# Performance work log

Hardware: AMD Instinct MI355X
Metric: run time of the kernel (lower is better)

## Reference

```python
import jax, jax.numpy as jnp
import numpy as np

U_DIM = 2048
V_DIM = 2048
LATENT = 2048
BATCH = 8192
SLOPE = 0.001  # LeakyReLU negative slope
EPS = 1e-5     # torch LayerNorm default eps


def layer_norm(x, gamma, beta):
    mu = jnp.mean(x, axis=-1, keepdims=True)
    var = jnp.var(x, axis=-1, keepdims=True)
    return (x - mu) * jax.lax.rsqrt(var + EPS) * gamma + beta


def leaky_relu(x):
    return jnp.where(x >= 0, x, SLOPE * x)


def setup_inputs() -> dict:
    key = jax.random.key(0)
    ks = jax.random.split(key, 6)
    u = jax.random.normal(ks[0], (BATCH, V_DIM), dtype=jnp.float32)
    v = jax.random.normal(ks[1], (BATCH, U_DIM), dtype=jnp.float32)
    # LayerNorm affine params (torch default: weight=1, bias=0 at init; randomize slightly)
    ln_u_w = jnp.ones((V_DIM,), jnp.float32)
    ln_u_b = jnp.zeros((V_DIM,), jnp.float32)
    ln_v_w = jnp.ones((U_DIM,), jnp.float32)
    ln_v_b = jnp.zeros((U_DIM,), jnp.float32)
    # Linear params (Kaiming-uniform-like scale)
    su = 1.0 / np.sqrt(V_DIM)
    sv = 1.0 / np.sqrt(U_DIM)
    W_u = jax.random.uniform(ks[2], (V_DIM, LATENT), jnp.float32, -su, su)
    b_u = jax.random.uniform(ks[3], (LATENT,), jnp.float32, -su, su)
    W_v = jax.random.uniform(ks[4], (U_DIM, LATENT), jnp.float32, -sv, sv)
    b_v = jax.random.uniform(ks[5], (LATENT,), jnp.float32, -sv, sv)
    return {"u": u, "v": v, "ln_u_w": ln_u_w, "ln_u_b": ln_u_b,
            "ln_v_w": ln_v_w, "ln_v_b": ln_v_b,
            "W_u": W_u, "b_u": b_u, "W_v": W_v, "b_v": b_v}


def reference(u, v, ln_u_w, ln_u_b, ln_v_w, ln_v_b, W_u, b_u, W_v, b_v):
    # u tower: LayerNorm -> Linear -> LeakyReLU
    hu = leaky_relu(layer_norm(u, ln_u_w, ln_u_b) @ W_u + b_u)   # [B, latent]
    # v tower: LayerNorm -> Linear -> LeakyReLU
    hv = leaky_relu(layer_norm(v, ln_v_w, ln_v_b) @ W_v + b_v)   # [B, latent]
    # dot-product reduction per row
    return jnp.sum(hu * hv, axis=-1)                              # [B]
```

## Files before the change

kernel.cpp:

```cpp
#include <hip/hip_runtime.h>

typedef unsigned short u16;
typedef __attribute__((ext_vector_type(8))) short short8;
typedef __attribute__((ext_vector_type(16))) float f32x16;

#define DIM 2048
#define NROWS 8192
#define SLOPE 0.001f
#define LN_EPS 1e-5f

#define LN_BLOCKS 4096
#define WT_BLOCKS 2048

#define BM 256
#define BN 256
#define BK 64
#define NT (DIM / BK)
#define TAUMAX (2 * NT)

__device__ __forceinline__ u16 f2bf(float f) {
    unsigned int u = __float_as_uint(f);
    u += 0x7FFFu + ((u >> 16) & 1u);
    return (u16)(u >> 16);
}

__device__ __forceinline__ void gload_lds16(const void* g, void* l) {
    __builtin_amdgcn_global_load_lds(
        (const __attribute__((address_space(1))) void*)g,
        (__attribute__((address_space(3))) void*)l, 16, 0, 0);
}

__global__ __launch_bounds__(256) void prep_kernel(
    const float* __restrict__ u, const float* __restrict__ v,
    const float* __restrict__ lnu_w, const float* __restrict__ lnu_b,
    const float* __restrict__ lnv_w, const float* __restrict__ lnv_b,
    const float* __restrict__ Wu, const float* __restrict__ Wv,
    u16* __restrict__ Au, u16* __restrict__ Av,
    u16* __restrict__ WtU, u16* __restrict__ WtV,
    float* __restrict__ out)
{
    __shared__ u16 tile[64][66];

    if (blockIdx.x < NROWS / 256)
        out[(blockIdx.x << 8) | threadIdx.x] = 0.f;

    if (blockIdx.x < LN_BLOCKS) {
        const int wave = threadIdx.x >> 6;
        const int lane = threadIdx.x & 63;
        const int r = blockIdx.x * 4 + wave;
        const bool isv = r >= NROWS;
        const int row = isv ? (r - NROWS) : r;
        const float* __restrict__ src = (isv ? v : u) + (size_t)row * DIM;
        const float* __restrict__ gw = isv ? lnv_w : lnu_w;
        const float* __restrict__ gb = isv ? lnv_b : lnu_b;
        u16* __restrict__ dst = (isv ? Av : Au) + (size_t)row * DIM;

        float4 x[8];
        #pragma unroll
        for (int i = 0; i < 8; ++i)
            x[i] = *(const float4*)(src + i * 256 + lane * 4);

        float s = 0.f, s2 = 0.f;
        #pragma unroll
        for (int i = 0; i < 8; ++i) {
            s  += (x[i].x + x[i].y) + (x[i].z + x[i].w);
            s2 += x[i].x*x[i].x + x[i].y*x[i].y + x[i].z*x[i].z + x[i].w*x[i].w;
        }
        #pragma unroll
        for (int m = 1; m < 64; m <<= 1) {
            s  += __shfl_xor(s, m);
            s2 += __shfl_xor(s2, m);
        }
        const float mu = s * (1.0f / DIM);
        const float rstd = rsqrtf(s2 * (1.0f / DIM) - mu * mu + LN_EPS);

        #pragma unroll
        for (int i = 0; i < 8; ++i) {
            const float4 w4 = *(const float4*)(gw + i * 256 + lane * 4);
            const float4 b4 = *(const float4*)(gb + i * 256 + lane * 4);
            union { u16 us[4]; uint2 v2; } pk;
            pk.us[0] = f2bf((x[i].x - mu) * rstd * w4.x + b4.x);
            pk.us[1] = f2bf((x[i].y - mu) * rstd * w4.y + b4.y);
            pk.us[2] = f2bf((x[i].z - mu) * rstd * w4.z + b4.z);
            pk.us[3] = f2bf((x[i].w - mu) * rstd * w4.w + b4.w);
            *(uint2*)(dst + i * 256 + lane * 4) = pk.v2;
        }
    } else {
        const int b = blockIdx.x - LN_BLOCKS;
        const int tower = b >> 10;
        const int t6 = b & 1023;
        const int n0 = (t6 & 31) * 64;
        const int k0 = (t6 >> 5) * 64;
        const float* __restrict__ src = tower ? Wv : Wu;
        u16* __restrict__ dst = tower ? WtV : WtU;
        const int c  = threadIdx.x & 15;
        const int rq = threadIdx.x >> 4;

        #pragma unroll
        for (int i = 0; i < 4; ++i) {
            const int k = rq + 16 * i;
            const float4 w = *(const float4*)(src + (size_t)(k0 + k) * DIM + n0 + c * 4);
            union { u16 us[4]; uint2 v2; } pk;
            pk.us[0] = f2bf(w.x); pk.us[1] = f2bf(w.y);
            pk.us[2] = f2bf(w.z); pk.us[3] = f2bf(w.w);
            *(uint2*)&tile[k][c * 4] = pk.v2;
        }
        __syncthreads();
        #pragma unroll
        for (int i = 0; i < 4; ++i) {
            const int n = rq + 16 * i;
            union { u16 us[4]; uint2 v2; } pk;
            #pragma unroll
            for (int j = 0; j < 4; ++j) pk.us[j] = tile[c * 4 + j][n];
            *(uint2*)(dst + (size_t)(n0 + n) * DIM + k0 + c * 4) = pk.v2;
        }
    }
}

__global__ __launch_bounds__(512) void fused_gemm_dot(
    const u16* __restrict__ Au, const u16* __restrict__ Av,
    const u16* __restrict__ WtU, const u16* __restrict__ WtV,
    const float* __restrict__ b_u, const float* __restrict__ b_v,
    uint4* __restrict__ Hu, float* __restrict__ out)
{
    __shared__ __align__(16) u16 smA[3][BM * BK];
    __shared__ __align__(16) u16 smB[2][BN * BK];

    const int tid   = threadIdx.x;
    const int wave  = tid >> 6;
    const int lane  = tid & 63;
    const int l31   = lane & 31;
    const int khalf = lane >> 5;
    const int wr    = wave >> 2;
    const int wc    = wave & 3;
    const int srow  = lane >> 3;
    const int gsw   = ((lane & 7) ^ srow ^ wave) * 8;

    const int bid = blockIdx.x;
    const int bn  = bid & 7;
    const int bm  = bid >> 3;
    const size_t arow0 = (size_t)bm * BM;
    const size_t ncol0 = (size_t)bn * BN;

#define STAGE_A(T, buf, h) do {                                                    \
        const u16* as_ = (((T) >= NT) ? Av : Au) + arow0 * DIM                     \
                         + (size_t)((T) & (NT - 1)) * BK;                          \
        _Pragma("unroll")                                                          \
        for (int i2_ = 0; i2_ < 2; ++i2_) {                                        \
            const int rg_ = (h) * 128 + i2_ * 64 + wave * 8;                       \
            gload_lds16(as_ + (size_t)(rg_ + srow) * DIM + gsw,                    \
                        &smA[buf][rg_ * BK]);                                      \
        }                                                                          \
    } while (0)

#define STAGE_B(T, h) do {                                                         \
        const u16* bs_ = (((T) >= NT) ? WtV : WtU) + ncol0 * DIM                   \
                         + (size_t)((T) & (NT - 1)) * BK;                          \
        _Pragma("unroll")                                                          \
        for (int i2_ = 0; i2_ < 2; ++i2_) {                                        \
            const int rg_ = (h) * 128 + i2_ * 64 + wave * 8;                       \
            gload_lds16(bs_ + (size_t)(rg_ + srow) * DIM + gsw,                    \
                        &smB[(T) & 1][rg_ * BK]);                                  \
        }                                                                          \
    } while (0)

#define PHASE(AB, BB, KS, STAGE_STMT) do {                                         \
        const u16* sa_ = &smA[AB][0];                                              \
        const u16* sb_ = &smB[BB][0];                                              \
        const int cb_ = (KS) * 2 + khalf;                                          \
        short8 af_[4], bf_[2];                                                     \
        _Pragma("unroll")                                                          \
        for (int mi_ = 0; mi_ < 4; ++mi_) {                                        \
            const int row_ = wr * 128 + mi_ * 32 + l31;                            \
            const int sl_ = cb_ ^ (row_ & 7) ^ ((row_ >> 3) & 7);                  \
            af_[mi_] = *(const short8*)(sa_ + row_ * BK + sl_ * 8);                \
        }                                                                          \
        _Pragma("unroll")                                                          \
        for (int ni_ = 0; ni_ < 2; ++ni_) {                                        \
            const int row_ = wc * 64 + ni_ * 32 + l31;                             \
            const int sl_ = cb_ ^ (row_ & 7) ^ ((row_ >> 3) & 7);                  \
            bf_[ni_] = *(const short8*)(sb_ + row_ * BK + sl_ * 8);                \
        }                                                                          \
        STAGE_STMT;                                                                \
        __builtin_amdgcn_s_barrier();                                              \
        asm volatile("s_waitcnt lgkmcnt(0)" ::: "memory");                         \
        __builtin_amdgcn_s_setprio(1);                                             \
        _Pragma("unroll")                                                          \
        for (int mi_ = 0; mi_ < 4; ++mi_)                                          \
            _Pragma("unroll")                                                      \
            for (int ni_ = 0; ni_ < 2; ++ni_)                                      \
                acc[mi_][ni_] = __builtin_amdgcn_mfma_f32_32x32x16_bf16(           \
                    af_[mi_], bf_[ni_], acc[mi_][ni_], 0, 0, 0);                   \
        __builtin_amdgcn_s_setprio(0);                                             \
    } while (0)

    f32x16 acc[4][2];

    #pragma unroll
    for (int mi = 0; mi < 4; ++mi)
        #pragma unroll
        for (int ni = 0; ni < 2; ++ni)
            #pragma unroll
            for (int r = 0; r < 16; ++r)
                acc[mi][ni][r] = 0.f;

    STAGE_A(0, 0, 0); STAGE_A(0, 0, 1);
    STAGE_B(0, 0);    STAGE_B(0, 1);
    STAGE_A(1, 1, 0); STAGE_A(1, 1, 1);
    asm volatile("s_waitcnt vmcnt(4)" ::: "memory");
    __builtin_amdgcn_s_barrier();
    asm volatile("" ::: "memory");

    int a0 = 0;
    #pragma unroll 1
    for (int i = 0; i < NT; ++i) {
        const int tau = 2 * i;
        const int a1 = (a0 + 1 < 3) ? a0 + 1 : a0 - 2;
        const int a2 = (a0 + 2 < 3) ? a0 + 2 : a0 - 1;

        PHASE(a0, 0, 0, { STAGE_B(tau + 1, 0); });
        __builtin_amdgcn_s_barrier();
        PHASE(a0, 0, 1, { STAGE_B(tau + 1, 1); });
        __builtin_amdgcn_s_barrier();
        PHASE(a0, 0, 2, { if (i < NT - 1) STAGE_A(tau + 2, a2, 0); });
        __builtin_amdgcn_s_barrier();
        PHASE(a0, 0, 3, { if (i < NT - 1) STAGE_A(tau + 2, a2, 1); });
        if (i < NT - 1) asm volatile("s_waitcnt vmcnt(4)" ::: "memory");
        else            asm volatile("s_waitcnt vmcnt(0)" ::: "memory");
        __builtin_amdgcn_s_barrier();
        asm volatile("" ::: "memory");

        PHASE(a1, 1, 0, { if (i < NT - 1) STAGE_B(tau + 2, 0); });
        __builtin_amdgcn_s_barrier();
        PHASE(a1, 1, 1, { if (i < NT - 1) STAGE_B(tau + 2, 1); });
        __builtin_amdgcn_s_barrier();
        PHASE(a1, 1, 2, { if (i < NT - 1) STAGE_A(tau + 3, a0, 0); });
        __builtin_amdgcn_s_barrier();
        PHASE(a1, 1, 3, { if (i < NT - 1) STAGE_A(tau + 3, a0, 1); });
        if (i < NT - 1) asm volatile("s_waitcnt vmcnt(4)" ::: "memory");
        __builtin_amdgcn_s_barrier();
        asm volatile("" ::: "memory");

        a0 = a2;

        if (i == 15) {
            #pragma unroll
            for (int mi = 0; mi < 4; ++mi) {
                #pragma unroll
                for (int ni = 0; ni < 2; ++ni) {
                    const float bias = b_u[ncol0 + wc * 64 + ni * 32 + l31];
                    unsigned pk[8];
                    #pragma unroll
                    for (int p = 0; p < 8; ++p) {
                        float h0 = acc[mi][ni][p * 2] + bias;
                        float h1 = acc[mi][ni][p * 2 + 1] + bias;
                        h0 = h0 >= 0.f ? h0 : SLOPE * h0;
                        h1 = h1 >= 0.f ? h1 : SLOPE * h1;
                        pk[p] = (unsigned)f2bf(h0) | ((unsigned)f2bf(h1) << 16);
                    }
                    Hu[((size_t)bid * 16 + mi * 4 + ni * 2 + 0) * 512 + tid] =
                        make_uint4(pk[0], pk[1], pk[2], pk[3]);
                    Hu[((size_t)bid * 16 + mi * 4 + ni * 2 + 1) * 512 + tid] =
                        make_uint4(pk[4], pk[5], pk[6], pk[7]);
                }
                #pragma unroll
                for (int ni = 0; ni < 2; ++ni)
                    #pragma unroll
                    for (int r = 0; r < 16; ++r) acc[mi][ni][r] = 0.f;
            }
        }
    }

    asm volatile("s_waitcnt vmcnt(0)" ::: "memory");
    #pragma unroll
    for (int mi = 0; mi < 4; ++mi) {
        union { uint4 v4[4]; unsigned w[16]; } hu;
        #pragma unroll
        for (int j = 0; j < 4; ++j)
            hu.v4[j] = Hu[((size_t)bid * 16 + mi * 4 + j) * 512 + tid];
        #pragma unroll
        for (int rg = 0; rg < 4; ++rg) {
            float rsum[4] = {0.f, 0.f, 0.f, 0.f};
            #pragma unroll
            for (int ni = 0; ni < 2; ++ni) {
                const float bias = b_v[ncol0 + wc * 64 + ni * 32 + l31];
                #pragma unroll
                for (int r = 0; r < 4; ++r) {
                    const int reg = rg * 4 + r;
                    float hv = acc[mi][ni][reg] + bias;
                    hv = hv >= 0.f ? hv : SLOPE * hv;
                    const unsigned pk = hu.w[ni * 8 + (reg >> 1)];
                    const unsigned bits = (reg & 1) ? (pk & 0xFFFF0000u) : (pk << 16);
                    rsum[r] += __uint_as_float(bits) * hv;
                }
            }
            #pragma unroll
            for (int r = 0; r < 4; ++r) {
                const int reg = rg * 4 + r;
                float vsum = rsum[r];
                vsum += __shfl_xor(vsum, 1);
                vsum += __shfl_xor(vsum, 2);
                vsum += __shfl_xor(vsum, 4);
                vsum += __shfl_xor(vsum, 8);
                vsum += __shfl_xor(vsum, 16);
                if (l31 == 0) {
                    const int row = (int)arow0 + wr * 128 + mi * 32
                                  + (reg & 3) + 8 * (reg >> 2) + 4 * khalf;
                    atomicAdd(out + row, vsum);
                }
            }
        }
    }
#undef STAGE_A
#undef STAGE_B
#undef PHASE
}

extern "C" void kernel_launch(void* const* d_in, const int* in_sizes, int n_in,
                              void* d_out, int out_size, void* d_ws, size_t ws_size,
                              hipStream_t stream)
{
    const float* u     = (const float*)d_in[0];
    const float* v     = (const float*)d_in[1];
    const float* lnu_w = (const float*)d_in[2];
    const float* lnu_b = (const float*)d_in[3];
    const float* lnv_w = (const float*)d_in[4];
    const float* lnv_b = (const float*)d_in[5];
    const float* W_u   = (const float*)d_in[6];
    const float* b_u   = (const float*)d_in[7];
    const float* W_v   = (const float*)d_in[8];
    const float* b_v   = (const float*)d_in[9];
    float* out = (float*)d_out;

    char* ws = (char*)d_ws;
    u16*  Au  = (u16*)(ws);
    u16*  Av  = (u16*)(ws + (size_t)NROWS * DIM * 2);
    u16*  WtU = (u16*)(ws + (size_t)NROWS * DIM * 4);
    u16*  WtV = (u16*)(ws + (size_t)NROWS * DIM * 4 + (size_t)DIM * DIM * 2);
    uint4* Hu = (uint4*)(ws + (size_t)NROWS * DIM * 4 + (size_t)DIM * DIM * 4);

    prep_kernel<<<LN_BLOCKS + WT_BLOCKS, 256, 0, stream>>>(
        u, v, lnu_w, lnu_b, lnv_w, lnv_b, W_u, W_v, Au, Av, WtU, WtV, out);
    fused_gemm_dot<<<dim3((NROWS / BM) * (DIM / BN)), 512, 0, stream>>>(
        Au, Av, WtU, WtV, b_u, b_v, Hu, out);
}
```

Before: 352.5 us.

## Split fused dual-tower GEMM into two templated single-tower kernel launches

Result: no change. 352.8 us (+0.1%).

```diff
diff --git a/kernel.cpp b/kernel.cpp
--- a/kernel.cpp
+++ b/kernel.cpp
@@ -15,8 +15,8 @@
 #define BM 256
 #define BN 256
 #define BK 64
-#define NT (DIM / BK)
-#define TAUMAX (2 * NT)
+#define NKT (DIM / BK)
+#define NIT (NKT / 2)
 
 __device__ __forceinline__ u16 f2bf(float f) {
     unsigned int u = __float_as_uint(f);
@@ -117,11 +117,11 @@
     }
 }
 
-__global__ __launch_bounds__(512) void fused_gemm_dot(
-    const u16* __restrict__ Au, const u16* __restrict__ Av,
-    const u16* __restrict__ WtU, const u16* __restrict__ WtV,
-    const float* __restrict__ b_u, const float* __restrict__ b_v,
-    uint4* __restrict__ Hu, float* __restrict__ out)
+template <bool DOT>
+__global__ __launch_bounds__(512) void tower_gemm(
+    const u16* __restrict__ A, const u16* __restrict__ Wt,
+    const float* __restrict__ bias_g, uint4* __restrict__ Hu,
+    float* __restrict__ out)
 {
     __shared__ __align__(16) u16 smA[3][BM * BK];
     __shared__ __align__(16) u16 smB[2][BN * BK];
@@ -143,8 +143,7 @@
     const size_t ncol0 = (size_t)bn * BN;
 
 #define STAGE_A(T, buf, h) do {                                                    \
-        const u16* as_ = (((T) >= NT) ? Av : Au) + arow0 * DIM                     \
-                         + (size_t)((T) & (NT - 1)) * BK;                          \
+        const u16* as_ = A + arow0 * DIM + (size_t)(T) * BK;                       \
         _Pragma("unroll")                                                          \
         for (int i2_ = 0; i2_ < 2; ++i2_) {                                        \
             const int rg_ = (h) * 128 + i2_ * 64 + wave * 8;                       \
@@ -154,8 +153,7 @@
     } while (0)
 
 #define STAGE_B(T, h) do {                                                         \
-        const u16* bs_ = (((T) >= NT) ? WtV : WtU) + ncol0 * DIM                   \
-                         + (size_t)((T) & (NT - 1)) * BK;                          \
+        const u16* bs_ = Wt + ncol0 * DIM + (size_t)(T) * BK;                      \
         _Pragma("unroll")                                                          \
         for (int i2_ = 0; i2_ < 2; ++i2_) {                                        \
             const int rg_ = (h) * 128 + i2_ * 64 + wave * 8;                       \
@@ -195,7 +193,6 @@
     } while (0)
 
     f32x16 acc[4][2];
-
     #pragma unroll
     for (int mi = 0; mi < 4; ++mi)
         #pragma unroll
@@ -213,7 +210,7 @@
 
     int a0 = 0;
     #pragma unroll 1
-    for (int i = 0; i < NT; ++i) {
+    for (int i = 0; i < NIT; ++i) {
         const int tau = 2 * i;
         const int a1 = (a0 + 1 < 3) ? a0 + 1 : a0 - 2;
         const int a2 = (a0 + 2 < 3) ? a0 + 2 : a0 - 1;
@@ -222,91 +219,86 @@
         __builtin_amdgcn_s_barrier();
         PHASE(a0, 0, 1, { STAGE_B(tau + 1, 1); });
         __builtin_amdgcn_s_barrier();
-        PHASE(a0, 0, 2, { if (i < NT - 1) STAGE_A(tau + 2, a2, 0); });
-        __builtin_amdgcn_s_barrier();
-        PHASE(a0, 0, 3, { if (i < NT - 1) STAGE_A(tau + 2, a2, 1); });
-        if (i < NT - 1) asm volatile("s_waitcnt vmcnt(4)" ::: "memory");
-        else            asm volatile("s_waitcnt vmcnt(0)" ::: "memory");
+        PHASE(a0, 0, 2, { if (i < NIT - 1) STAGE_A(tau + 2, a2, 0); });
+        __builtin_amdgcn_s_barrier();
+        PHASE(a0, 0, 3, { if (i < NIT - 1) STAGE_A(tau + 2, a2, 1); });
+        if (i < NIT - 1) asm volatile("s_waitcnt vmcnt(4)" ::: "memory");
+        else             asm volatile("s_waitcnt vmcnt(0)" ::: "memory");
         __builtin_amdgcn_s_barrier();
         asm volatile("" ::: "memory");
 
-        PHASE(a1, 1, 0, { if (i < NT - 1) STAGE_B(tau + 2, 0); });
-        __builtin_amdgcn_s_barrier();
-        PHASE(a1, 1, 1, { if (i < NT - 1) STAGE_B(tau + 2, 1); });
-        __builtin_amdgcn_s_barrier();
-        PHASE(a1, 1, 2, { if (i < NT - 1) STAGE_A(tau + 3, a0, 0); });
-        __builtin_amdgcn_s_barrier();
-        PHASE(a1, 1, 3, { if (i < NT - 1) STAGE_A(tau + 3, a0, 1); });
-        if (i < NT - 1) asm volatile("s_waitcnt vmcnt(4)" ::: "memory");
+        PHASE(a1, 1, 0, { if (i < NIT - 1) STAGE_B(tau + 2, 0); });
+        __builtin_amdgcn_s_barrier();
+        PHASE(a1, 1, 1, { if (i < NIT - 1) STAGE_B(tau + 2, 1); });
+        __builtin_amdgcn_s_barrier();
+        PHASE(a1, 1, 2, { if (i < NIT - 1) STAGE_A(tau + 3, a0, 0); });
+        __builtin_amdgcn_s_barrier();
+        PHASE(a1, 1, 3, { if (i < NIT - 1) STAGE_A(tau + 3, a0, 1); });
+        if (i < NIT - 1) asm volatile("s_waitcnt vmcnt(4)" ::: "memory");
         __builtin_amdgcn_s_barrier();
         asm volatile("" ::: "memory");
 
         a0 = a2;
-
-        if (i == 15) {
-            #pragma unroll
-            for (int mi = 0; mi < 4; ++mi) {
+    }
+
+    if constexpr (!DOT) {
+        #pragma unroll
+        for (int mi = 0; mi < 4; ++mi) {
+            #pragma unroll
+            for (int ni = 0; ni < 2; ++ni) {
+                const float bias = bias_g[ncol0 + wc * 64 + ni * 32 + l31];
+                unsigned pk[8];
+                #pragma unroll
+                for (int p = 0; p < 8; ++p) {
+                    float h0 = acc[mi][ni][p * 2] + bias;
+                    float h1 = acc[mi][ni][p * 2 + 1] + bias;
+                    h0 = h0 >= 0.f ? h0 : SLOPE * h0;
+                    h1 = h1 >= 0.f ? h1 : SLOPE * h1;
+                    pk[p] = (unsigned)f2bf(h0) | ((unsigned)f2bf(h1) << 16);
+                }
+                Hu[((size_t)bid * 16 + mi * 4 + ni * 2 + 0) * 512 + tid] =
+                    make_uint4(pk[0], pk[1], pk[2], pk[3]);
+                Hu[((size_t)bid * 16 + mi * 4 + ni * 2 + 1) * 512 + tid] =
+                    make_uint4(pk[4], pk[5], pk[6], pk[7]);
+            }
+        }
+    } else {
+        #pragma unroll
+        for (int mi = 0; mi < 4; ++mi) {
+            union { uint4 v4[4]; unsigned w[16]; } hu;
+            #pragma unroll
+            for (int j = 0; j < 4; ++j)
+                hu.v4[j] = Hu[((size_t)bid * 16 + mi * 4 + j) * 512 + tid];
+            #pragma unroll
+            for (int rg = 0; rg < 4; ++rg) {
+                float rsum[4] = {0.f, 0.f, 0.f, 0.f};
                 #pragma unroll
                 for (int ni = 0; ni < 2; ++ni) {
-                    const float bias = b_u[ncol0 + wc * 64 + ni * 32 + l31];
-                    unsigned pk[8];
+                    const float bias = bias_g[ncol0 + wc * 64 + ni * 32 + l31];
                     #pragma unroll
-                    for (int p = 0; p < 8; ++p) {
-                        float h0 = acc[mi][ni][p * 2] + bias;
-                        float h1 = acc[mi][ni][p * 2 + 1] + bias;
-                        h0 = h0 >= 0.f ? h0 : SLOPE * h0;
-                        h1 = h1 >= 0.f ? h1 : SLOPE * h1;
-                        pk[p] = (unsigned)f2bf(h0) | ((unsigned)f2bf(h1) << 16);
+                    for (int r = 0; r < 4; ++r) {
+                        const int reg = rg * 4 + r;
+                        float hv = acc[mi][ni][reg] + bias;
+                        hv = hv >= 0.f ? hv : SLOPE * hv;
+                        const unsigned pk = hu.w[ni * 8 + (reg >> 1)];
+                        const unsigned bits = (reg & 1) ? (pk & 0xFFFF0000u) : (pk << 16);
+                        rsum[r] += __uint_as_float(bits) * hv;
                     }
-                    Hu[((size_t)bid * 16 + mi * 4 + ni * 2 + 0) * 512 + tid] =
-                        make_uint4(pk[0], pk[1], pk[2], pk[3]);
-                    Hu[((size_t)bid * 16 + mi * 4 + ni * 2 + 1) * 512 + tid] =
-                        make_uint4(pk[4], pk[5], pk[6], pk[7]);
                 }
-                #pragma unroll
-                for (int ni = 0; ni < 2; ++ni)
-                    #pragma unroll
-                    for (int r = 0; r < 16; ++r) acc[mi][ni][r] = 0.f;
-            }
-        }
-    }
-
-    asm volatile("s_waitcnt vmcnt(0)" ::: "memory");
-    #pragma unroll
-    for (int mi = 0; mi < 4; ++mi) {
-        union { uint4 v4[4]; unsigned w[16]; } hu;
-        #pragma unroll
-        for (int j = 0; j < 4; ++j)
-            hu.v4[j] = Hu[((size_t)bid * 16 + mi * 4 + j) * 512 + tid];
-        #pragma unroll
-        for (int rg = 0; rg < 4; ++rg) {
-            float rsum[4] = {0.f, 0.f, 0.f, 0.f};
-            #pragma unroll
-            for (int ni = 0; ni < 2; ++ni) {
-                const float bias = b_v[ncol0 + wc * 64 + ni * 32 + l31];
                 #pragma unroll
                 for (int r = 0; r < 4; ++r) {
                     const int reg = rg * 4 + r;
-                    float hv = acc[mi][ni][reg] + bias;
-                    hv = hv >= 0.f ? hv : SLOPE * hv;
-                    const unsigned pk = hu.w[ni * 8 + (reg >> 1)];
-                    const unsigned bits = (reg & 1) ? (pk & 0xFFFF0000u) : (pk << 16);
-                    rsum[r] += __uint_as_float(bits) * hv;
-                }
-            }
-            #pragma unroll
-            for (int r = 0; r < 4; ++r) {
-                const int reg = rg * 4 + r;
-                float vsum = rsum[r];
-                vsum += __shfl_xor(vsum, 1);
-                vsum += __shfl_xor(vsum, 2);
-                vsum += __shfl_xor(vsum, 4);
-                vsum += __shfl_xor(vsum, 8);
-                vsum += __shfl_xor(vsum, 16);
-                if (l31 == 0) {
-                    const int row = (int)arow0 + wr * 128 + mi * 32
-                                  + (reg & 3) + 8 * (reg >> 2) + 4 * khalf;
-                    atomicAdd(out + row, vsum);
+                    float vsum = rsum[r];
+                    vsum += __shfl_xor(vsum, 1);
+                    vsum += __shfl_xor(vsum, 2);
+                    vsum += __shfl_xor(vsum, 4);
+                    vsum += __shfl_xor(vsum, 8);
+                    vsum += __shfl_xor(vsum, 16);
+                    if (l31 == 0) {
+                        const int row = (int)arow0 + wr * 128 + mi * 32
+                                      + (reg & 3) + 8 * (reg >> 2) + 4 * khalf;
+                        atomicAdd(out + row, vsum);
+                    }
                 }
             }
         }
@@ -341,6 +333,6 @@
 
     prep_kernel<<<LN_BLOCKS + WT_BLOCKS, 256, 0, stream>>>(
         u, v, lnu_w, lnu_b, lnv_w, lnv_b, W_u, W_v, Au, Av, WtU, WtV, out);
-    fused_gemm_dot<<<dim3((NROWS / BM) * (DIM / BN)), 512, 0, stream>>>(
-        Au, Av, WtU, WtV, b_u, b_v, Hu, out);
-}
+    tower_gemm<false><<<256, 512, 0, stream>>>(Au, WtU, b_u, Hu, nullptr);
+    tower_gemm<true ><<<256, 512, 0, stream>>>(Av, WtV, b_v, Hu, out);
+}
```
